# Optimization experiments

Hardware: AMD Instinct MI355X
Metric: run time of the kernel (lower is better)

The kernel has to match this reference:

```python
import jax, jax.numpy as jnp
import numpy as np

B, N, D_IN = 8, 1024, 512
H, D_HEAD = 8, 64
D_EXPAND, D_OUT = 2048, 512
D_Q = D_HEAD * H            # 512
D_V = D_IN * H              # 4096
D_QKV = 2 * D_Q + D_V       # 5120
EPS = 1e-5


def setup_inputs() -> dict:
    key = jax.random.key(0)
    ks = jax.random.split(key, 16)
    s = 0.02
    return {
        "x": jax.random.normal(ks[0], (B, N, D_IN), jnp.float32),
        "pos_enc": jax.random.normal(ks[1], (1, N, D_IN), jnp.float32),
        "gamma1": jnp.ones((1, 1, D_IN), jnp.float32),
        "beta1": jnp.zeros((1, 1, D_IN), jnp.float32),
        "scale": jnp.asarray(1.414, jnp.float32),
        "W_qkv": jax.random.normal(ks[2], (D_IN, D_QKV), jnp.float32) * s,
        "b_qkv": jax.random.normal(ks[3], (D_QKV,), jnp.float32) * s,
        "W_merge": jax.random.normal(ks[4], (D_V, D_IN), jnp.float32) * s,
        "b_merge": jax.random.normal(ks[5], (D_IN,), jnp.float32) * s,
        "gamma2": jnp.ones((1, 1, D_IN), jnp.float32),
        "beta2": jnp.zeros((1, 1, D_IN), jnp.float32),
        "W1": jax.random.normal(ks[6], (D_IN, D_EXPAND), jnp.float32) * s,
        "b1": jax.random.normal(ks[7], (D_EXPAND,), jnp.float32) * s,
        "gamma3": jnp.ones((1, 1, D_EXPAND), jnp.float32),
        "beta3": jnp.zeros((1, 1, D_EXPAND), jnp.float32),
        "W2": jax.random.normal(ks[8], (D_EXPAND, D_OUT), jnp.float32) * s,
        "b2": jax.random.normal(ks[9], (D_OUT,), jnp.float32) * s,
    }


def _feature_norm(x, gamma, beta):
    # torch FeatureNorm: stats over dim=1 (sequence dim), unbiased=False
    mean = x.mean(axis=1, keepdims=True)
    var = x.var(axis=1, keepdims=True)
    return gamma * (x - mean) / jnp.sqrt(var + EPS) + beta


def _swish(x):
    return x * jax.nn.sigmoid(x)


def reference(x, pos_enc, gamma1, beta1, scale, W_qkv, b_qkv, W_merge, b_merge,
              gamma2, beta2, W1, b1, gamma3, beta3, W2, b2):
    Bs, Ns, _ = x.shape
    h = _feature_norm(x, gamma1, beta1) + pos_enc
    qkv = _swish(h) @ W_qkv + b_qkv                      # (B, N, D_QKV)
    q = qkv[..., :D_Q].reshape(Bs, Ns, H, D_HEAD).transpose(0, 2, 1, 3)        # (B,H,N,dh)
    k = qkv[..., D_Q:2 * D_Q].reshape(Bs, Ns, H, D_HEAD).transpose(0, 2, 1, 3)
    v = qkv[..., 2 * D_Q:].reshape(Bs, Ns, H, D_IN).transpose(0, 2, 1, 3)      # (B,H,N,d_in)
    # squared euclidean distance via |q|^2 + |k|^2 - 2 q.k
    q2 = jnp.sum(q * q, axis=-1)                         # (B,H,N)
    k2 = jnp.sum(k * k, axis=-1)                         # (B,H,N)
    qk = jnp.einsum('bhnc,bhmc->bhnm', q, k)             # (B,H,N,N)
    d2 = jnp.maximum(q2[..., :, None] + k2[..., None, :] - 2.0 * qk, 0.0)
    score = jnp.exp(-d2 / (scale * scale))               # RBF kernel, no softmax
    out = jnp.einsum('bhnm,bhmc->bhnc', score, v)        # (B,H,N,d_in)
    out = out.transpose(0, 2, 1, 3).reshape(Bs, Ns, H * D_IN)
    x2 = x + out @ W_merge + b_merge                     # merge heads + residual
    ffh = _feature_norm(x2, gamma2, beta2) @ W1 + b1
    ffh = _swish(_feature_norm(ffh, gamma3, beta3))
    ff = ffh @ W2 + b2
    return ff + x2                                        # shortcut is Identity (d_in == d_out)
```

## Files before the change

kernel.cpp:

```cpp
#include <hip/hip_runtime.h>
#include <hip/hip_bf16.h>
#include <stdint.h>

typedef __bf16 bf16_t;
typedef __bf16 bf16x8 __attribute__((ext_vector_type(8)));
typedef __bf16 bf16x4 __attribute__((ext_vector_type(4)));
typedef float f32x4 __attribute__((ext_vector_type(4)));

__global__ void transp_kernel(const float* __restrict__ in, bf16_t* __restrict__ out,
                              int K, int N) {
  __shared__ float tile[32][33];
  int k0 = blockIdx.x * 32, n0 = blockIdx.y * 32;
  int tx = threadIdx.x, ty = threadIdx.y;
#pragma unroll
  for (int i = 0; i < 4; i++)
    tile[ty + 8 * i][tx] = in[(size_t)(k0 + ty + 8 * i) * N + n0 + tx];
  __syncthreads();
#pragma unroll
  for (int i = 0; i < 4; i++)
    out[(size_t)(n0 + ty + 8 * i) * K + k0 + tx] = (bf16_t)tile[tx][ty + 8 * i];
}

#define NSPLIT 16

template <typename T>
__global__ __launch_bounds__(256) void norm_partial(
    const T* __restrict__ in, float* __restrict__ part, int D) {
  const int nd = D >> 7;
  const int bid = blockIdx.x;
  const int s = bid % NSPLIT;
  const int rem = bid / NSPLIT;
  const int dc = rem % nd;
  const int b = rem / nd;
  const int t = threadIdx.x;
  const int d = (dc << 7) + (t & 127);
  const int half = t >> 7;
  const int rows = 1024 / NSPLIT;
  const T* base = in + ((size_t)b * 1024 + s * rows) * D + d;
  float sum = 0.f, sq = 0.f;
  for (int n = half; n < rows; n += 2) {
    float v = (float)base[(size_t)n * D];
    sum += v;
    sq += v * v;
  }
  __shared__ float r0[256], r1[256];
  r0[t] = sum;
  r1[t] = sq;
  __syncthreads();
  if (t < 128) {
    float ssum = r0[t] + r0[t + 128];
    float ssq = r1[t] + r1[t + 128];
    size_t col = (size_t)b * D + (dc << 7) + t;
    part[col * (2 * NSPLIT) + s] = ssum;
    part[col * (2 * NSPLIT) + NSPLIT + s] = ssq;
  }
}

__global__ __launch_bounds__(256) void norm_stats(
    const float* __restrict__ part, float2* __restrict__ stats, int total) {
  int col = blockIdx.x * 256 + threadIdx.x;
  if (col >= total) return;
  const float* p = part + (size_t)col * (2 * NSPLIT);
  float sum = 0.f, sq = 0.f;
#pragma unroll
  for (int s = 0; s < NSPLIT; s++) {
    sum += p[s];
    sq += p[NSPLIT + s];
  }
  float mean = sum * (1.f / 1024.f);
  float var = sq * (1.f / 1024.f) - mean * mean;
  stats[col] = make_float2(mean, rsqrtf(var + 1e-5f));
}

template <int MODE, typename T>
__global__ __launch_bounds__(256) void norm_apply(
    const T* __restrict__ in, const float2* __restrict__ stats,
    const float* __restrict__ gamma, const float* __restrict__ beta,
    const float* __restrict__ pos, bf16_t* __restrict__ out, int logD) {
  const int D = 1 << logD;
  size_t idx = ((size_t)blockIdx.x * 256 + threadIdx.x) * 4;
  int d = (int)(idx & (D - 1));
  size_t row = idx >> logD;
  int b = (int)(row >> 10);
  int n = (int)(row & 1023);
  float vv[4];
  if constexpr (sizeof(T) == 4) {
    float4 v = *(const float4*)(in + idx);
    vv[0] = v.x; vv[1] = v.y; vv[2] = v.z; vv[3] = v.w;
  } else {
    bf16x4 v = *(const bf16x4*)(in + idx);
#pragma unroll
    for (int j = 0; j < 4; j++) vv[j] = (float)v[j];
  }
  float4 g = *(const float4*)(gamma + d);
  float4 be = *(const float4*)(beta + d);
  const float2* st = stats + (size_t)b * D + d;
  float gg[4] = {g.x, g.y, g.z, g.w};
  float bb[4] = {be.x, be.y, be.z, be.w};
  float pp[4] = {0.f, 0.f, 0.f, 0.f};
  if (MODE == 1) {
    float4 p = *(const float4*)(pos + (size_t)n * D + d);
    pp[0] = p.x; pp[1] = p.y; pp[2] = p.z; pp[3] = p.w;
  }
  bf16x4 o;
#pragma unroll
  for (int j = 0; j < 4; j++) {
    float2 s = st[j];
    float h = gg[j] * (vv[j] - s.x) * s.y + bb[j];
    if (MODE == 1) h += pp[j];
    if (MODE == 1 || MODE == 3) h = h / (1.f + __expf(-h));
    o[j] = (bf16_t)h;
  }
  *(bf16x4*)(out + idx) = o;
}

__global__ __launch_bounds__(256) void combine2(
    const float* __restrict__ p0, const float* __restrict__ p1,
    const float* __restrict__ bias, const float* __restrict__ res,
    float* __restrict__ out) {
  size_t idx = ((size_t)blockIdx.x * 256 + threadIdx.x) * 4;
  int col = (int)(idx & 511);
  float4 a = *(const float4*)(p0 + idx);
  float4 b = *(const float4*)(p1 + idx);
  float4 rr = *(const float4*)(res + idx);
  float4 bi = *(const float4*)(bias + col);
  float4 o;
  o.x = a.x + b.x + rr.x + bi.x;
  o.y = a.y + b.y + rr.y + bi.y;
  o.z = a.z + b.z + rr.z + bi.z;
  o.w = a.w + b.w + rr.w + bi.w;
  *(float4*)(out + idx) = o;
}

enum { EPI_QKV = 0, EPI_RAW = 1, EPI_BF16 = 2 };

template <int EPI, int SPLITK>
__global__ void __launch_bounds__(256, 2) gemm_bf16(
    const bf16_t* __restrict__ A, const bf16_t* __restrict__ Bt,
    const float* __restrict__ bias,
    void* __restrict__ out0, bf16_t* __restrict__ out1,
    int M, int N, int K) {
  __shared__ bf16_t smem[2 * 128 * 64];
  bf16_t* sA = smem;
  bf16_t* sB = smem + 128 * 64;
  const int nwg = gridDim.x;
  int wg = blockIdx.x;
  wg = (wg & 7) * (nwg >> 3) + (wg >> 3);
  int kslice = 0;
  if (SPLITK) {
    int half = nwg >> 1;
    kslice = (wg >= half) ? 1 : 0;
    wg -= kslice * half;
  }
  const int mt = M >> 7;
  const int bm = wg % mt;
  const int bn = wg / mt;
  const int t = threadIdx.x;
  const int w = t >> 6, l = t & 63;
  const int wm = w >> 1, wn = w & 1;
  const int lrow = l >> 3;
  const int lcol = (l & 7) ^ lrow;

  f32x4 acc[4][4];
  const f32x4 z4 = {0.f, 0.f, 0.f, 0.f};
#pragma unroll
  for (int m = 0; m < 4; m++)
#pragma unroll
    for (int n = 0; n < 4; n++) acc[m][n] = z4;

  const bf16_t* Asrc = A + (size_t)(bm * 128 + w * 32 + lrow) * K + lcol * 8;
  const bf16_t* Bsrc = Bt + (size_t)(bn * 128 + w * 32 + lrow) * K + lcol * 8;

  const int kbeg = SPLITK ? kslice * (K >> 1) : 0;
  const int kend = kbeg + (SPLITK ? (K >> 1) : K);
  for (int kk = kbeg; kk < kend; kk += 64) {
#pragma unroll
    for (int i = 0; i < 4; i++) {
      __builtin_amdgcn_global_load_lds(
          (const __attribute__((address_space(1))) void*)(const void*)(Asrc + (size_t)i * 8 * K + kk),
          (__attribute__((address_space(3))) void*)(void*)((char*)sA + (w * 4 + i) * 1024),
          16, 0, 0);
      __builtin_amdgcn_global_load_lds(
          (const __attribute__((address_space(1))) void*)(const void*)(Bsrc + (size_t)i * 8 * K + kk),
          (__attribute__((address_space(3))) void*)(void*)((char*)sB + (w * 4 + i) * 1024),
          16, 0, 0);
    }
    __syncthreads();
#pragma unroll
    for (int ks = 0; ks < 2; ks++) {
      bf16x8 af[4], bfr[4];
      const int lc = ks * 4 + (l >> 4);
#pragma unroll
      for (int m = 0; m < 4; m++) {
        int row = wm * 64 + m * 16 + (l & 15);
        af[m] = *(const bf16x8*)((const char*)sA + row * 128 + ((lc ^ (row & 7)) << 4));
      }
#pragma unroll
      for (int n = 0; n < 4; n++) {
        int row = wn * 64 + n * 16 + (l & 15);
        bfr[n] = *(const bf16x8*)((const char*)sB + row * 128 + ((lc ^ (row & 7)) << 4));
      }
      __builtin_amdgcn_s_setprio(1);
#pragma unroll
      for (int m = 0; m < 4; m++)
#pragma unroll
        for (int n = 0; n < 4; n++)
          acc[m][n] = __builtin_amdgcn_mfma_f32_16x16x32_bf16(af[m], bfr[n], acc[m][n], 0, 0, 0);
      __builtin_amdgcn_s_setprio(0);
    }
    __syncthreads();
  }

  const int rowbase = bm * 128 + wm * 64 + ((l >> 4) << 2);
  const int colbase = bn * 128 + wn * 64 + (l & 15);
#pragma unroll
  for (int m = 0; m < 4; m++) {
#pragma unroll
    for (int n = 0; n < 4; n++) {
      int row = rowbase + m * 16;
      int col = colbase + n * 16;
      if (EPI == EPI_QKV) {
        float bc = bias[col];
        if (col < 1024) {
          bf16_t* qkb = (bf16_t*)out0;
#pragma unroll
          for (int r = 0; r < 4; r++)
            qkb[(size_t)(row + r) * 1024 + col] = (bf16_t)(acc[m][n][r] + bc);
        } else {
          int c2 = col - 1024;
          int hh = c2 >> 9, vc = c2 & 511;
          int bidx = row >> 10, nidx = row & 1023;
          bf16x4 pk;
#pragma unroll
          for (int r = 0; r < 4; r++) pk[r] = (bf16_t)(acc[m][n][r] + bc);
          *(bf16x4*)(out1 + ((size_t)((bidx << 3) + hh) * 512 + vc) * 1024 + nidx) = pk;
        }
      } else if (EPI == EPI_RAW) {
        float* o = (float*)out0 + (size_t)kslice * M * N;
#pragma unroll
        for (int r = 0; r < 4; r++) o[(size_t)(row + r) * N + col] = acc[m][n][r];
      } else {
        float bc = bias[col];
#pragma unroll
        for (int r = 0; r < 4; r++)
          out1[(size_t)(row + r) * N + col] = (bf16_t)(acc[m][n][r] + bc);
      }
    }
  }
}

__global__ void q2k2_kernel(const bf16_t* __restrict__ qk, float* __restrict__ q2,
                            float* __restrict__ k2) {
  int tid = blockIdx.x * 256 + threadIdx.x;
  int b = tid >> 13;
  int h = (tid >> 10) & 7;
  int n = tid & 1023;
  const bf16_t* row = qk + (size_t)((b << 10) + n) * 1024 + (h << 6);
  float sq = 0.f, sk = 0.f;
#pragma unroll
  for (int i = 0; i < 8; i++) {
    bf16x8 vq = *(const bf16x8*)(row + i * 8);
    bf16x8 vk = *(const bf16x8*)(row + 512 + i * 8);
#pragma unroll
    for (int j = 0; j < 8; j++) {
      float fq = (float)vq[j];
      sq += fq * fq;
      float fk = (float)vk[j];
      sk += fk * fk;
    }
  }
  q2[tid] = sq;
  k2[tid] = sk;
}

__global__ void __launch_bounds__(256, 2) attn_kernel(
    const bf16_t* __restrict__ qk, const bf16_t* __restrict__ vt,
    const float* __restrict__ q2, const float* __restrict__ k2,
    const float* __restrict__ scale_p, bf16_t* __restrict__ attn_out) {
  __shared__ bf16_t s_lds[64 * 64];
  const int blk = blockIdx.x;
  const int bh = (blk & 7) * 8 + (blk >> 7);
  const int mtile = (blk >> 3) & 15;
  const int b = bh >> 3, h = bh & 7;
  const int t = threadIdx.x, w = t >> 6, l = t & 63;
  const float sc = scale_p[0];
  const float minus_inv = -1.f / (sc * sc);

  const bf16_t* qbase = qk + ((size_t)((b << 10) + (mtile << 6))) * 1024 + (h << 6);
  bf16x8 qf[4][2];
#pragma unroll
  for (int it = 0; it < 4; it++)
#pragma unroll
    for (int kc = 0; kc < 2; kc++)
      qf[it][kc] = *(const bf16x8*)(qbase + (size_t)(it * 16 + (l & 15)) * 1024 +
                                    kc * 32 + ((l >> 4) << 3));
  float q2r[4];
  const float* q2base = q2 + (bh << 10) + (mtile << 6);
#pragma unroll
  for (int it = 0; it < 4; it++) q2r[it] = q2base[it * 16 + (l & 15)];

  f32x4 acc[4][8];
  const f32x4 z4 = {0.f, 0.f, 0.f, 0.f};
#pragma unroll
  for (int m = 0; m < 4; m++)
#pragma unroll
    for (int nn = 0; nn < 8; nn++) acc[m][nn] = z4;

  const bf16_t* kbase = qk + ((size_t)(b << 10)) * 1024 + 512 + (h << 6);
  const bf16_t* vbase = vt + ((size_t)(bh << 9)) * 1024;
  const float* k2base = k2 + (bh << 10);

  for (int kt = 0; kt < 16; kt++) {
    float k2r[4];
#pragma unroll
    for (int r = 0; r < 4; r++)
      k2r[r] = k2base[kt * 64 + w * 16 + ((l >> 4) << 2) + r];
    f32x4 sacc[4];
#pragma unroll
    for (int it = 0; it < 4; it++) sacc[it] = z4;
#pragma unroll
    for (int kc = 0; kc < 2; kc++) {
      bf16x8 kf = *(const bf16x8*)(kbase + (size_t)(kt * 64 + w * 16 + (l & 15)) * 1024 +
                                   kc * 32 + ((l >> 4) << 3));
      __builtin_amdgcn_s_setprio(1);
#pragma unroll
      for (int it = 0; it < 4; it++)
        sacc[it] = __builtin_amdgcn_mfma_f32_16x16x32_bf16(kf, qf[it][kc], sacc[it], 0, 0, 0);
      __builtin_amdgcn_s_setprio(0);
    }
    __syncthreads();
#pragma unroll
    for (int it = 0; it < 4; it++) {
      int i = it * 16 + (l & 15);
      bf16x4 pk;
#pragma unroll
      for (int r = 0; r < 4; r++) {
        float d2 = fmaxf(q2r[it] + k2r[r] - 2.f * sacc[it][r], 0.f);
        pk[r] = (bf16_t)__expf(d2 * minus_inv);
      }
      int jc8 = (w << 2) + (l >> 4);
      *(bf16x4*)((char*)s_lds + i * 128 + ((jc8 ^ ((i & 7) << 1)) << 3)) = pk;
    }
    __syncthreads();
#pragma unroll
    for (int kc = 0; kc < 2; kc++) {
      bf16x8 sf[4];
#pragma unroll
      for (int m = 0; m < 4; m++) {
        int i = m * 16 + (l & 15);
        int jcA = (kc << 3) + ((l >> 4) << 1);
        sf[m] = *(const bf16x8*)((const char*)s_lds + i * 128 +
                                 ((jcA ^ ((i & 7) << 1)) << 3));
      }
      bf16x8 vf[8];
#pragma unroll
      for (int nn = 0; nn < 8; nn++)
        vf[nn] = *(const bf16x8*)(vbase + (size_t)(w * 128 + nn * 16 + (l & 15)) * 1024 +
                                  kt * 64 + (kc << 5) + ((l >> 4) << 3));
      __builtin_amdgcn_s_setprio(1);
#pragma unroll
      for (int nn = 0; nn < 8; nn++)
#pragma unroll
        for (int m = 0; m < 4; m++)
          acc[m][nn] = __builtin_amdgcn_mfma_f32_16x16x32_bf16(sf[m], vf[nn], acc[m][nn], 0, 0, 0);
      __builtin_amdgcn_s_setprio(0);
    }
  }
#pragma unroll
  for (int m = 0; m < 4; m++) {
    int nidx = (mtile << 6) + m * 16 + ((l >> 4) << 2);
#pragma unroll
    for (int nn = 0; nn < 8; nn++) {
      int col = (h << 9) + w * 128 + nn * 16 + (l & 15);
      bf16_t* o = attn_out + ((size_t)((b << 10) + nidx)) * 4096 + col;
#pragma unroll
      for (int r = 0; r < 4; r++) o[(size_t)r * 4096] = (bf16_t)acc[m][nn][r];
    }
  }
}

extern "C" void kernel_launch(void* const* d_in, const int* in_sizes, int n_in,
                              void* d_out, int out_size, void* d_ws, size_t ws_size,
                              hipStream_t stream) {
  const float* x    = (const float*)d_in[0];
  const float* pos  = (const float*)d_in[1];
  const float* g1   = (const float*)d_in[2];
  const float* be1  = (const float*)d_in[3];
  const float* scl  = (const float*)d_in[4];
  const float* Wqkv = (const float*)d_in[5];
  const float* bqkv = (const float*)d_in[6];
  const float* Wmrg = (const float*)d_in[7];
  const float* bmrg = (const float*)d_in[8];
  const float* g2   = (const float*)d_in[9];
  const float* be2  = (const float*)d_in[10];
  const float* W1   = (const float*)d_in[11];
  const float* b1   = (const float*)d_in[12];
  const float* g3   = (const float*)d_in[13];
  const float* be3  = (const float*)d_in[14];
  const float* W2   = (const float*)d_in[15];
  const float* b2   = (const float*)d_in[16];
  float* outp = (float*)d_out;

  char* ws = (char*)d_ws;
  size_t off = 0;
  auto alloc = [&](size_t bytes) {
    char* p = ws + off;
    off += (bytes + 255) & ~(size_t)255;
    return p;
  };
  bf16_t* wtq = (bf16_t*)alloc(5120ull * 512 * 2);
  bf16_t* wtm = (bf16_t*)alloc(512ull * 4096 * 2);
  bf16_t* wt1 = (bf16_t*)alloc(2048ull * 512 * 2);
  bf16_t* wt2 = (bf16_t*)alloc(512ull * 2048 * 2);
  float*  q2  = (float*)alloc(65536ull * 4);
  float*  k2  = (float*)alloc(65536ull * 4);
  float*  prt = (float*)alloc(16384ull * 2 * NSPLIT * 4);
  float2* sts = (float2*)alloc(16384ull * 8);
  bf16_t* swh = (bf16_t*)alloc(8192ull * 512 * 2);
  bf16_t* qkb = (bf16_t*)alloc(8192ull * 1024 * 2);
  float*  x2b = (float*)alloc(8192ull * 512 * 4);
  bf16_t* x2n = (bf16_t*)alloc(8192ull * 512 * 2);
  bf16_t* atn = (bf16_t*)alloc(8192ull * 4096 * 2);
  bf16_t* vtb = (bf16_t*)alloc(64ull * 512 * 1024 * 2);
  float*  pmg = (float*)vtb;
  bf16_t* ffh = (bf16_t*)vtb;
  float*  pff = (float*)(vtb + 8192ull * 2048);
  bf16_t* ffn = (bf16_t*)atn;

  dim3 tb(32, 8);
  transp_kernel<<<dim3(512 / 32, 5120 / 32), tb, 0, stream>>>(Wqkv, wtq, 512, 5120);
  transp_kernel<<<dim3(4096 / 32, 512 / 32), tb, 0, stream>>>(Wmrg, wtm, 4096, 512);
  transp_kernel<<<dim3(512 / 32, 2048 / 32), tb, 0, stream>>>(W1, wt1, 512, 2048);
  transp_kernel<<<dim3(2048 / 32, 512 / 32), tb, 0, stream>>>(W2, wt2, 2048, 512);

  norm_partial<float><<<8 * 4 * NSPLIT, 256, 0, stream>>>(x, prt, 512);
  norm_stats<<<16, 256, 0, stream>>>(prt, sts, 8 * 512);
  norm_apply<1, float><<<4096, 256, 0, stream>>>(x, sts, g1, be1, pos, swh, 9);

  gemm_bf16<EPI_QKV, 0><<<64 * 40, 256, 0, stream>>>(swh, wtq, bqkv,
                                                     (void*)qkb, vtb, 8192, 5120, 512);
  q2k2_kernel<<<256, 256, 0, stream>>>(qkb, q2, k2);
  attn_kernel<<<1024, 256, 0, stream>>>(qkb, vtb, q2, k2, scl, atn);

  gemm_bf16<EPI_RAW, 1><<<2 * 64 * 4, 256, 0, stream>>>(atn, wtm, nullptr,
                                                        (void*)pmg, nullptr, 8192, 512, 4096);
  combine2<<<4096, 256, 0, stream>>>(pmg, pmg + 8192ull * 512, bmrg, x, x2b);

  norm_partial<float><<<8 * 4 * NSPLIT, 256, 0, stream>>>(x2b, prt, 512);
  norm_stats<<<16, 256, 0, stream>>>(prt, sts, 8 * 512);
  norm_apply<2, float><<<4096, 256, 0, stream>>>(x2b, sts, g2, be2, nullptr, x2n, 9);

  gemm_bf16<EPI_BF16, 0><<<64 * 16, 256, 0, stream>>>(x2n, wt1, b1,
                                                      nullptr, ffh, 8192, 2048, 512);

  norm_partial<bf16_t><<<8 * 16 * NSPLIT, 256, 0, stream>>>(ffh, prt, 2048);
  norm_stats<<<64, 256, 0, stream>>>(prt, sts, 8 * 2048);
  norm_apply<3, bf16_t><<<16384, 256, 0, stream>>>(ffh, sts, g3, be3, nullptr, ffn, 11);

  gemm_bf16<EPI_RAW, 1><<<2 * 64 * 4, 256, 0, stream>>>(ffn, wt2, nullptr,
                                                        (void*)pff, nullptr, 8192, 512, 2048);
  combine2<<<4096, 256, 0, stream>>>(pff, pff + 8192ull * 512, b2, x2b, outp);
}
```

Measured before the change: 549.2 us.

## Software-pipeline attention loop with double-buffered score tile in LDS

The RBF attention kernel now double-buffers the 64x64 score tile in LDS. It computes the next tile's QK^T scores while running the PV MFMAs on the current tile, then writes the exp results into the other buffer. This removes one of the two barriers per iteration and lets score computation overlap the PV matmul. In exchange it doubles the LDS used for scores, keeps more live registers for sacc across pv_tile, and drops the setprio hints around the QK MFMAs.

Result: slower. 590.0 us (+7.4%).

```diff
diff --git a/kernel.cpp b/kernel.cpp
--- a/kernel.cpp
+++ b/kernel.cpp
@@ -277,7 +277,7 @@
     const bf16_t* __restrict__ qk, const bf16_t* __restrict__ vt,
     const float* __restrict__ q2, const float* __restrict__ k2,
     const float* __restrict__ scale_p, bf16_t* __restrict__ attn_out) {
-  __shared__ bf16_t s_lds[64 * 64];
+  __shared__ bf16_t s_lds[2][64 * 64];
   const int blk = blockIdx.x;
   const int bh = (blk & 7) * 8 + (blk >> 7);
   const int mtile = (blk >> 3) & 15;
@@ -310,25 +310,23 @@
   const bf16_t* vbase = vt + ((size_t)(bh << 9)) * 1024;
   const float* k2base = k2 + (bh << 10);
 
-  for (int kt = 0; kt < 16; kt++) {
-    float k2r[4];
+  auto qk_tile = [&](int kt, f32x4* sacc, float* k2r) {
 #pragma unroll
     for (int r = 0; r < 4; r++)
       k2r[r] = k2base[kt * 64 + w * 16 + ((l >> 4) << 2) + r];
-    f32x4 sacc[4];
 #pragma unroll
     for (int it = 0; it < 4; it++) sacc[it] = z4;
 #pragma unroll
     for (int kc = 0; kc < 2; kc++) {
       bf16x8 kf = *(const bf16x8*)(kbase + (size_t)(kt * 64 + w * 16 + (l & 15)) * 1024 +
                                    kc * 32 + ((l >> 4) << 3));
-      __builtin_amdgcn_s_setprio(1);
 #pragma unroll
       for (int it = 0; it < 4; it++)
         sacc[it] = __builtin_amdgcn_mfma_f32_16x16x32_bf16(kf, qf[it][kc], sacc[it], 0, 0, 0);
-      __builtin_amdgcn_s_setprio(0);
-    }
-    __syncthreads();
+    }
+  };
+  auto exp_write = [&](const f32x4* sacc, const float* k2r, int buf) {
+    char* sb = (char*)&s_lds[buf][0];
 #pragma unroll
     for (int it = 0; it < 4; it++) {
       int i = it * 16 + (l & 15);
@@ -339,9 +337,11 @@
         pk[r] = (bf16_t)__expf(d2 * minus_inv);
       }
       int jc8 = (w << 2) + (l >> 4);
-      *(bf16x4*)((char*)s_lds + i * 128 + ((jc8 ^ ((i & 7) << 1)) << 3)) = pk;
-    }
-    __syncthreads();
+      *(bf16x4*)(sb + i * 128 + ((jc8 ^ ((i & 7) << 1)) << 3)) = pk;
+    }
+  };
+  auto pv_tile = [&](int kt, int buf) {
+    const char* sb = (const char*)&s_lds[buf][0];
 #pragma unroll
     for (int kc = 0; kc < 2; kc++) {
       bf16x8 sf[4];
@@ -349,8 +349,7 @@
       for (int m = 0; m < 4; m++) {
         int i = m * 16 + (l & 15);
         int jcA = (kc << 3) + ((l >> 4) << 1);
-        sf[m] = *(const bf16x8*)((const char*)s_lds + i * 128 +
-                                 ((jcA ^ ((i & 7) << 1)) << 3));
+        sf[m] = *(const bf16x8*)(sb + i * 128 + ((jcA ^ ((i & 7) << 1)) << 3));
       }
       bf16x8 vf[8];
 #pragma unroll
@@ -365,7 +364,29 @@
           acc[m][nn] = __builtin_amdgcn_mfma_f32_16x16x32_bf16(sf[m], vf[nn], acc[m][nn], 0, 0, 0);
       __builtin_amdgcn_s_setprio(0);
     }
-  }
+  };
+
+  {
+    f32x4 sacc[4];
+    float k2r[4];
+    qk_tile(0, sacc, k2r);
+    exp_write(sacc, k2r, 0);
+  }
+  __syncthreads();
+
+  int cur = 0;
+#pragma unroll 1
+  for (int kt = 0; kt < 15; kt++) {
+    f32x4 sacc[4];
+    float k2r[4];
+    qk_tile(kt + 1, sacc, k2r);
+    pv_tile(kt, cur);
+    exp_write(sacc, k2r, cur ^ 1);
+    __syncthreads();
+    cur ^= 1;
+  }
+  pv_tile(15, cur);
+
 #pragma unroll
   for (int m = 0; m < 4; m++) {
     int nidx = (mtile << 6) + m * 16 + ((l >> 4) << 2);
```
